# Kernel tuning notes

Hardware: AMD Instinct MI355X
Metric: run time of the kernel (lower is better)

Reference implementation:

```python
import jax, jax.numpy as jnp
import numpy as np
import math

D_MODEL = 512
N_HEADS = 8
WINDOW = 32
B, L, S = 4, 2048, 2048


def setup_inputs() -> dict:
    key = jax.random.key(0)
    ks = jax.random.split(key, 12)
    scale = 1.0 / math.sqrt(D_MODEL)
    inp = {
        "queries": jax.random.normal(ks[0], (B, L, D_MODEL), jnp.float32),
        "keys": jax.random.normal(ks[1], (B, S, D_MODEL), jnp.float32),
        "values": jax.random.normal(ks[2], (B, S, D_MODEL), jnp.float32),
        # TriangularCausalMask: True above the diagonal => masked
        "attn_mask": jnp.triu(jnp.ones((L, S), jnp.bool_), k=1)[None, None],
        "Wq": jax.random.normal(ks[3], (D_MODEL, D_MODEL), jnp.float32) * scale,
        "bq": jnp.zeros((D_MODEL,), jnp.float32),
        "Wk": jax.random.normal(ks[4], (D_MODEL, D_MODEL), jnp.float32) * scale,
        "bk": jnp.zeros((D_MODEL,), jnp.float32),
        "Wv": jax.random.normal(ks[5], (D_MODEL, D_MODEL), jnp.float32) * scale,
        "bv": jnp.zeros((D_MODEL,), jnp.float32),
        "Wo": jax.random.normal(ks[6], (D_MODEL, D_MODEL), jnp.float32) * scale,
        "bo": jnp.zeros((D_MODEL,), jnp.float32),
        "gamma": jnp.ones((1,), jnp.float32) * 0.5,
    }
    return inp


def reference(queries, keys, values, attn_mask, Wq, bq, Wk, bk, Wv, bv, Wo, bo, gamma):
    Bq, Lq, _ = queries.shape
    Sq = keys.shape[1]
    H = N_HEADS
    q = (queries @ Wq + bq).reshape(Bq, Lq, H, -1)  # [B,L,H,dk]
    k = (keys @ Wk + bk).reshape(Bq, Sq, H, -1)
    v = (values @ Wv + bv).reshape(Bq, Sq, H, -1)

    scores = jnp.einsum('blhd,bshd->bhls', q, k) / math.sqrt(D_MODEL)  # [B,H,L,S]

    # exponential decay on relative position
    rel = jnp.arange(Lq)[:, None] - jnp.arange(Sq)[None, :]  # [L,S]
    decay = jnp.exp(-gamma[0] * jnp.abs(rel).astype(scores.dtype))
    scores = scores * decay[None, None]

    # sliding-window mask (exact replica of _create_window_mask)
    t = jnp.arange(Lq)
    start = jnp.clip(t - WINDOW // 2, 0, None)
    end = jnp.clip(t + WINDOW // 2 + 1, None, Sq)
    wmask = (t[:, None] >= start[None, :]) & (t[:, None] < end[None, :])  # [L,S]
    neg_inf = jnp.asarray(-jnp.inf, scores.dtype)
    scores = jnp.where(wmask[None, None], scores, neg_inf)

    # causal mask: True = masked
    scores = jnp.where(attn_mask, neg_inf, scores)

    attn = jax.nn.softmax(scores, axis=-1)  # dropout is identity at eval
    context = jnp.einsum('bhls,bshd->blhd', attn, v).reshape(Bq, Lq, -1)
    out = context @ Wo + bo
    return (out, attn)
```

## Files before the change

kernel.cpp:

```cpp
#include <hip/hip_runtime.h>
#include <hip/hip_bf16.h>
#include <cstdint>
#include <cstddef>

#define D_MODEL 512
#define N_HEADS 8
#define HDIM 64
#define SEQ 2048
#define B_SZ 4
#define M_TOT (B_SZ * SEQ)
#define ATTN_ROWS (B_SZ * N_HEADS * SEQ)
#define PROJ_ELEMS ((size_t)M_TOT * D_MODEL)

typedef __bf16 bf16x8 __attribute__((ext_vector_type(8)));
typedef float  f32x4  __attribute__((ext_vector_type(4)));

__device__ __forceinline__ unsigned short f2bf(float x) {
    __bf16 b = (__bf16)x;
    return __builtin_bit_cast(unsigned short, b);
}
__device__ __forceinline__ float bf2f(unsigned short u) {
    __bf16 b = __builtin_bit_cast(__bf16, u);
    return (float)b;
}

struct TransArgs {
    const float* W[4];
    unsigned short* Wt[4];
};

__global__ void transpose_k(TransArgs ta) {
    __shared__ float tile[32][33];
    const int z = blockIdx.z;
    const float* W = ta.W[z];
    unsigned short* Wt = ta.Wt[z];
    int x = blockIdx.x * 32 + threadIdx.x;
    int y0 = blockIdx.y * 32;
    for (int j = threadIdx.y; j < 32; j += 8)
        tile[j][threadIdx.x] = W[(size_t)(y0 + j) * D_MODEL + x];
    __syncthreads();
    int xo = blockIdx.y * 32 + threadIdx.x;
    int yo0 = blockIdx.x * 32;
    for (int j = threadIdx.y; j < 32; j += 8)
        Wt[(size_t)(yo0 + j) * D_MODEL + xo] = f2bf(tile[threadIdx.x][j]);
}

#define LDSTRIDE 72

template <int F32OUT>
__device__ __forceinline__ void gemm_tile(
    const float* __restrict__ A, const unsigned short* __restrict__ Wt,
    const float* __restrict__ bias, void* __restrict__ C,
    int m0, int n0, unsigned short* lsA, unsigned short* lsB) {
    const int tid = threadIdx.x;
    const int lane = tid & 63;
    const int wid = tid >> 6;
    const int wm = (wid >> 1) * 64;
    const int wn = (wid & 1) * 64;
    const int lrow = lane & 15;
    const int quad = lane >> 4;

    f32x4 acc[4][4];
#pragma unroll
    for (int i = 0; i < 4; ++i)
#pragma unroll
        for (int j = 0; j < 4; ++j)
            acc[i][j] = (f32x4){0.f, 0.f, 0.f, 0.f};

    for (int kt = 0; kt < D_MODEL; kt += 64) {
        __syncthreads();
#pragma unroll
        for (int p = 0; p < 4; ++p) {
            int c = p * 256 + tid;
            int r = c >> 3;
            int col = (c & 7) << 3;
            const float* src = &A[(size_t)(m0 + r) * D_MODEL + kt + col];
            float4 a0 = *(const float4*)src;
            float4 a1 = *(const float4*)(src + 4);
            unsigned short t8[8];
            t8[0] = f2bf(a0.x); t8[1] = f2bf(a0.y); t8[2] = f2bf(a0.z); t8[3] = f2bf(a0.w);
            t8[4] = f2bf(a1.x); t8[5] = f2bf(a1.y); t8[6] = f2bf(a1.z); t8[7] = f2bf(a1.w);
            *(uint4*)&lsA[r * LDSTRIDE + col] = *(const uint4*)t8;
        }
#pragma unroll
        for (int p = 0; p < 4; ++p) {
            int c = p * 256 + tid;
            int r = c >> 3;
            int col = (c & 7) << 3;
            *(uint4*)&lsB[r * LDSTRIDE + col] =
                *(const uint4*)&Wt[(size_t)(n0 + r) * D_MODEL + kt + col];
        }
        __syncthreads();
#pragma unroll
        for (int ks = 0; ks < 2; ++ks) {
            const int ko = ks * 32 + quad * 8;
            bf16x8 af[4], bfr[4];
#pragma unroll
            for (int mt = 0; mt < 4; ++mt)
                af[mt] = *(const bf16x8*)&lsA[(wm + mt * 16 + lrow) * LDSTRIDE + ko];
#pragma unroll
            for (int nt = 0; nt < 4; ++nt)
                bfr[nt] = *(const bf16x8*)&lsB[(wn + nt * 16 + lrow) * LDSTRIDE + ko];
#pragma unroll
            for (int mt = 0; mt < 4; ++mt)
#pragma unroll
                for (int nt = 0; nt < 4; ++nt)
                    acc[mt][nt] = __builtin_amdgcn_mfma_f32_16x16x32_bf16(
                        af[mt], bfr[nt], acc[mt][nt], 0, 0, 0);
        }
    }

#pragma unroll
    for (int nt = 0; nt < 4; ++nt) {
        const int gcol = n0 + wn + nt * 16 + lrow;
        const float bv = bias[gcol];
#pragma unroll
        for (int mt = 0; mt < 4; ++mt) {
            const int grow = m0 + wm + mt * 16 + quad * 4;
#pragma unroll
            for (int r = 0; r < 4; ++r) {
                const float v = acc[mt][nt][r] + bv;
                if (F32OUT)
                    __builtin_nontemporal_store(
                        v, &((float*)C)[(size_t)(grow + r) * D_MODEL + gcol]);
                else
                    ((unsigned short*)C)[(size_t)(grow + r) * D_MODEL + gcol] = f2bf(v);
            }
        }
    }
}

struct GemmArgs {
    const float* A[3];
    const unsigned short* Wt[3];
    const float* bias[3];
    void* C[3];
};

__global__ __launch_bounds__(256, 2) void gemm_qkv(GemmArgs ga) {
    __shared__ __align__(16) unsigned short lsA[128 * LDSTRIDE];
    __shared__ __align__(16) unsigned short lsB[128 * LDSTRIDE];
    const int f = blockIdx.x;
    const int z = f >> 8;
    const int xt = ((f >> 5) & 7) * 8 + (f & 7);
    const int yt = (f >> 3) & 3;
    gemm_tile<0>(ga.A[z], ga.Wt[z], ga.bias[z], ga.C[z], xt * 128, yt * 128, lsA, lsB);
}

#define KV_ROWS 80
#define LROW 72

__device__ __forceinline__ void load16f(const unsigned short* p, float* out) {
    bf16x8 a = *(const bf16x8*)p;
    bf16x8 b = *(const bf16x8*)(p + 8);
#pragma unroll
    for (int i = 0; i < 8; ++i) { out[i] = (float)a[i]; out[8 + i] = (float)b[i]; }
}

__global__ __launch_bounds__(256, 4) void attn3_k(
    const unsigned short* __restrict__ Q,
    const unsigned short* __restrict__ K,
    const unsigned short* __restrict__ V,
    const float* __restrict__ gamma_p,
    float* __restrict__ pb,
    float* __restrict__ ctx) {
    __shared__ __align__(16) unsigned short lk[KV_ROWS * LROW];
    __shared__ __align__(16) unsigned short lv[KV_ROWS * LROW];

    const int bh = blockIdx.y;
    const int t0 = blockIdx.x * 64;
    const int b = bh >> 3;
    const int h = bh & 7;
    const int tid = threadIdx.x;
    const int w = tid >> 6;
    const int lane = tid & 63;
    const int r = lane >> 2;
    const int c = lane & 3;

    const float g = gamma_p[0];
    const float rs = 0.044194173824159216f;

    const size_t srcbase = (size_t)b * SEQ * D_MODEL + (size_t)h * HDIM;
    for (int idx = tid; idx < KV_ROWS * 8; idx += 256) {
        const int row = idx >> 3;
        const int ch = (idx & 7) * 8;
        const int grow = t0 - 16 + row;
        uint4 kv4 = {0, 0, 0, 0};
        uint4 vv4 = {0, 0, 0, 0};
        if (grow >= 0) {
            const size_t off = srcbase + (size_t)grow * D_MODEL + ch;
            kv4 = *(const uint4*)&K[off];
            vv4 = *(const uint4*)&V[off];
        }
        *(uint4*)&lk[row * LROW + ch] = kv4;
        *(uint4*)&lv[row * LROW + ch] = vv4;
    }
    __syncthreads();

    const int gr = t0 + w * 16 + r;
    const size_t qoff = srcbase + (size_t)gr * D_MODEL + c * 16;
    float qv[16];
    load16f(&Q[qoff], qv);

    const int lr0 = w * 16 + r;
    float scr[17];
#pragma unroll
    for (int j = 0; j < 17; ++j) {
        float kvv[16];
        load16f(&lk[(lr0 + j) * LROW + c * 16], kvv);
        float part = 0.f;
#pragma unroll
        for (int i = 0; i < 16; ++i) part = fmaf(qv[i], kvv[i], part);
        part += __shfl_xor(part, 1, 64);
        part += __shfl_xor(part, 2, 64);
        const float dec = __expf(-g * (float)(16 - j));
        scr[j] = part * rs * dec;
        if (gr - 16 + j < 0) scr[j] = -__builtin_inff();
    }

    float m = scr[0];
#pragma unroll
    for (int j = 1; j < 17; ++j) m = fmaxf(m, scr[j]);
    float l = 0.f;
#pragma unroll
    for (int j = 0; j < 17; ++j) { scr[j] = __expf(scr[j] - m); l += scr[j]; }
    const float inv = 1.f / l;

    float acc[16];
#pragma unroll
    for (int i = 0; i < 16; ++i) acc[i] = 0.f;
#pragma unroll
    for (int j = 0; j < 17; ++j) {
        float vv[16];
        load16f(&lv[(lr0 + j) * LROW + c * 16], vv);
#pragma unroll
        for (int i = 0; i < 16; ++i) acc[i] = fmaf(scr[j], vv[i], acc[i]);
    }

    float* cp = &ctx[qoff];
#pragma unroll
    for (int i = 0; i < 16; i += 4) {
        f32x4 v = {acc[i] * inv, acc[i + 1] * inv, acc[i + 2] * inv, acc[i + 3] * inv};
        *(f32x4*)&cp[i] = v;
    }

    float* prow = &pb[((size_t)bh * SEQ + gr) * 20];
    for (int j = c; j < 17; j += 4) prow[j] = scr[j] * inv;
}

__global__ __launch_bounds__(256, 2) void fused_k(
    const float* __restrict__ Ctx,
    const unsigned short* __restrict__ WoT,
    const float* __restrict__ bo,
    float* __restrict__ out_p,
    const float* __restrict__ pb,
    float* __restrict__ attn_out) {
    __shared__ __align__(16) unsigned short lsA[128 * LDSTRIDE];
    __shared__ __align__(16) unsigned short lsB[128 * LDSTRIDE];

    if (blockIdx.x < 256) {
        const int f = blockIdx.x;
        const int xt = ((f >> 5) & 7) * 8 + (f & 7);
        const int yt = (f >> 3) & 3;
        gemm_tile<1>(Ctx, WoT, bo, out_p, xt * 128, yt * 128, lsA, lsB);
        return;
    }

    const int wb = blockIdx.x - 256;
    const int bh = wb >> 5;
    const int t0 = (wb & 31) * 64;
    const int tid = threadIdx.x;

    const size_t rowbase = ((size_t)bh * SEQ + t0) * SEQ;
    const size_t prowbase = ((size_t)bh * SEQ + t0) * 20;
    for (int i = tid; i < 64 * 512; i += 256) {
        const int row = i >> 9;
        const int c4 = i & 511;
        const int t = t0 + row;
        const int s_lo = (t - 16 < 0) ? 0 : t - 16;
        const int lo4 = s_lo >> 2;
        const int hi4 = t >> 2;
        f32x4 v = {0.f, 0.f, 0.f, 0.f};
        if ((unsigned)(c4 - lo4) <= (unsigned)(hi4 - lo4)) {
            const float* prow = &pb[prowbase + (size_t)row * 20];
            const int col0 = c4 * 4;
#pragma unroll
            for (int k = 0; k < 4; ++k) {
                const int col = col0 + k;
                v[k] = (col >= s_lo && col <= t) ? prow[col - (t - 16)] : 0.f;
            }
        }
        __builtin_nontemporal_store(
            v, (f32x4*)&attn_out[rowbase + (size_t)row * SEQ + (c4 << 2)]);
    }
}

extern "C" void kernel_launch(void* const* d_in, const int* in_sizes, int n_in,
                              void* d_out, int out_size, void* d_ws, size_t ws_size,
                              hipStream_t stream) {
    const float* queries = (const float*)d_in[0];
    const float* keys    = (const float*)d_in[1];
    const float* values  = (const float*)d_in[2];
    const float* Wq = (const float*)d_in[4];
    const float* bq = (const float*)d_in[5];
    const float* Wk = (const float*)d_in[6];
    const float* bk = (const float*)d_in[7];
    const float* Wv = (const float*)d_in[8];
    const float* bv = (const float*)d_in[9];
    const float* Wo = (const float*)d_in[10];
    const float* bo = (const float*)d_in[11];
    const float* gamma = (const float*)d_in[12];

    char* ws = (char*)d_ws;
    unsigned short* Qp  = (unsigned short*)ws;
    unsigned short* Kp  = Qp + PROJ_ELEMS;
    unsigned short* Vp  = Kp + PROJ_ELEMS;
    unsigned short* WT  = Vp + PROJ_ELEMS;
    unsigned short* WqT = WT;
    unsigned short* WkT = WT + 262144;
    unsigned short* WvT = WT + 2 * 262144;
    unsigned short* WoT = WT + 3 * 262144;
    float* Ctx = (float*)(WT + 4 * 262144);
    float* pb  = Ctx + PROJ_ELEMS;

    float* out_p  = (float*)d_out;
    float* attn_p = out_p + PROJ_ELEMS;

    TransArgs ta;
    ta.W[0] = Wq;  ta.W[1] = Wk;  ta.W[2] = Wv;  ta.W[3] = Wo;
    ta.Wt[0] = WqT; ta.Wt[1] = WkT; ta.Wt[2] = WvT; ta.Wt[3] = WoT;
    transpose_k<<<dim3(16, 16, 4), dim3(32, 8), 0, stream>>>(ta);

    GemmArgs gq;
    gq.A[0] = queries; gq.A[1] = keys;  gq.A[2] = values;
    gq.Wt[0] = WqT;    gq.Wt[1] = WkT;  gq.Wt[2] = WvT;
    gq.bias[0] = bq;   gq.bias[1] = bk; gq.bias[2] = bv;
    gq.C[0] = Qp;      gq.C[1] = Kp;    gq.C[2] = Vp;
    gemm_qkv<<<768, 256, 0, stream>>>(gq);

    attn3_k<<<dim3(SEQ / 64, B_SZ * N_HEADS), 256, 0, stream>>>(
        Qp, Kp, Vp, gamma, pb, Ctx);

    fused_k<<<1280, 256, 0, stream>>>(Ctx, WoT, bo, out_p, pb, attn_p);
}
```

Measured before the change: 651.4 us.

## Move attention-matrix zero fill into QKV GEMM launch and write only window band later

```diff
diff --git a/kernel.cpp b/kernel.cpp
--- a/kernel.cpp
+++ b/kernel.cpp
@@ -18,10 +18,6 @@
 __device__ __forceinline__ unsigned short f2bf(float x) {
     __bf16 b = (__bf16)x;
     return __builtin_bit_cast(unsigned short, b);
-}
-__device__ __forceinline__ float bf2f(unsigned short u) {
-    __bf16 b = __builtin_bit_cast(__bf16, u);
-    return (float)b;
 }
 
 struct TransArgs {
@@ -137,14 +133,23 @@
     void* C[3];
 };
 
-__global__ __launch_bounds__(256, 2) void gemm_qkv(GemmArgs ga) {
+__global__ __launch_bounds__(256, 2) void qkv_fill_k(GemmArgs ga, float* __restrict__ attn_p) {
     __shared__ __align__(16) unsigned short lsA[128 * LDSTRIDE];
     __shared__ __align__(16) unsigned short lsB[128 * LDSTRIDE];
-    const int f = blockIdx.x;
-    const int z = f >> 8;
-    const int xt = ((f >> 5) & 7) * 8 + (f & 7);
-    const int yt = (f >> 3) & 3;
-    gemm_tile<0>(ga.A[z], ga.Wt[z], ga.bias[z], ga.C[z], xt * 128, yt * 128, lsA, lsB);
+    if (blockIdx.x < 768) {
+        const int f = blockIdx.x;
+        const int z = f >> 8;
+        const int xt = ((f >> 5) & 7) * 8 + (f & 7);
+        const int yt = (f >> 3) & 3;
+        gemm_tile<0>(ga.A[z], ga.Wt[z], ga.bias[z], ga.C[z], xt * 128, yt * 128, lsA, lsB);
+        return;
+    }
+    const size_t n4 = (size_t)ATTN_ROWS * SEQ / 4;
+    const size_t stride = (size_t)1024 * 256;
+    size_t i = (size_t)(blockIdx.x - 768) * 256 + threadIdx.x;
+    f32x4 z = {0.f, 0.f, 0.f, 0.f};
+    for (; i < n4; i += stride)
+        __builtin_nontemporal_store(z, (f32x4*)attn_p + i);
 }
 
 #define KV_ROWS 80
@@ -266,32 +271,22 @@
         return;
     }
 
-    const int wb = blockIdx.x - 256;
-    const int bh = wb >> 5;
-    const int t0 = (wb & 31) * 64;
-    const int tid = threadIdx.x;
-
-    const size_t rowbase = ((size_t)bh * SEQ + t0) * SEQ;
-    const size_t prowbase = ((size_t)bh * SEQ + t0) * 20;
-    for (int i = tid; i < 64 * 512; i += 256) {
-        const int row = i >> 9;
-        const int c4 = i & 511;
-        const int t = t0 + row;
-        const int s_lo = (t - 16 < 0) ? 0 : t - 16;
-        const int lo4 = s_lo >> 2;
-        const int hi4 = t >> 2;
+    const int row = (blockIdx.x - 256) * 256 + threadIdx.x;
+    const int t = row & (SEQ - 1);
+    const int s_lo = (t - 16 < 0) ? 0 : t - 16;
+    const int lo4 = s_lo >> 2;
+    const int hi4 = t >> 2;
+    const float* prow = &pb[(size_t)row * 20];
+    float* dst = &attn_out[(size_t)row * SEQ];
+    for (int c4 = lo4; c4 <= hi4; ++c4) {
+        const int col0 = c4 * 4;
         f32x4 v = {0.f, 0.f, 0.f, 0.f};
-        if ((unsigned)(c4 - lo4) <= (unsigned)(hi4 - lo4)) {
-            const float* prow = &pb[prowbase + (size_t)row * 20];
-            const int col0 = c4 * 4;
-#pragma unroll
-            for (int k = 0; k < 4; ++k) {
-                const int col = col0 + k;
-                v[k] = (col >= s_lo && col <= t) ? prow[col - (t - 16)] : 0.f;
-            }
-        }
-        __builtin_nontemporal_store(
-            v, (f32x4*)&attn_out[rowbase + (size_t)row * SEQ + (c4 << 2)]);
+#pragma unroll
+        for (int k = 0; k < 4; ++k) {
+            const int col = col0 + k;
+            v[k] = (col >= s_lo && col <= t) ? prow[col - (t - 16)] : 0.f;
+        }
+        __builtin_nontemporal_store(v, (f32x4*)&dst[col0]);
     }
 }
 
@@ -336,10 +331,10 @@
     gq.Wt[0] = WqT;    gq.Wt[1] = WkT;  gq.Wt[2] = WvT;
     gq.bias[0] = bq;   gq.bias[1] = bk; gq.bias[2] = bv;
     gq.C[0] = Qp;      gq.C[1] = Kp;    gq.C[2] = Vp;
-    gemm_qkv<<<768, 256, 0, stream>>>(gq);
+    qkv_fill_k<<<1792, 256, 0, stream>>>(gq, attn_p);
 
     attn3_k<<<dim3(SEQ / 64, B_SZ * N_HEADS), 256, 0, stream>>>(
         Qp, Kp, Vp, gamma, pb, Ctx);
 
-    fused_k<<<1280, 256, 0, stream>>>(Ctx, WoT, bo, out_p, pb, attn_p);
-}
+    fused_k<<<512, 256, 0, stream>>>(Ctx, WoT, bo, out_p, pb, attn_p);
+}
```

Result: slower. 673.1 us (+3.3%).
